# Kernel optimization log

Hardware: AMD Instinct MI355X
Metric: run time of the kernel (lower is better)

The kernel has to match this reference:

```python
import jax, jax.numpy as jnp
import numpy as np

NUM_HEADS = 16


def setup_inputs() -> dict:
    key = jax.random.key(0)
    k1, k2, k3 = jax.random.split(key, 3)
    B, S, D = 4, 2048, 1024
    hidden_states = jax.random.normal(k1, (B, S, D), dtype=jnp.float32)
    w_qkv = jax.random.normal(k2, (D, 3 * D), dtype=jnp.float32) * (1.0 / np.sqrt(D))
    w_out = jax.random.normal(k3, (D, D), dtype=jnp.float32) * (1.0 / np.sqrt(D))
    return {"hidden_states": hidden_states, "w_qkv": w_qkv, "w_out": w_out}


def reference(hidden_states, w_qkv, w_out):
    B, S, D = hidden_states.shape
    H = NUM_HEADS
    d = D // H
    # fused QKV projection: [B, S, 3D] -> [3, B, S, H, d]
    qkv = (hidden_states @ w_qkv).reshape(B, S, 3, H, d)
    q, k, v = jnp.moveaxis(qkv, 2, 0)  # each [B, S, H, d]
    scale = 1.0 / np.sqrt(d).astype(np.float32)
    scores = jnp.einsum("bqhd,bkhd->bhqk", q, k) * scale  # [B, H, S, S]
    attn = jax.nn.softmax(scores, axis=-1)
    ctx = jnp.einsum("bhqk,bkhd->bqhd", attn, v).reshape(B, S, D)
    return ctx @ w_out
```

## Files before the change

### kernel.cpp

```cpp
#include <hip/hip_runtime.h>
#include <hip/hip_bf16.h>
#include <math.h>

typedef __bf16 bf16;
typedef __bf16 bf16x4 __attribute__((ext_vector_type(4)));
typedef __bf16 bf16x8 __attribute__((ext_vector_type(8)));
typedef float  f32x4  __attribute__((ext_vector_type(4)));

#define B_  4
#define S_  2048
#define D_  1024
#define H_  16
#define DH  64
#define M_  (B_*S_)
#define BH_ (B_*H_)

#define QSCALE 0.18033688011112042f

__device__ __forceinline__ void glds16(const bf16* g, bf16* l) {
  __builtin_amdgcn_global_load_lds((const __attribute__((address_space(1))) void*)g,
                                   (__attribute__((address_space(3))) void*)l, 16, 0, 0);
}

__global__ __launch_bounds__(256) void prep(const float* __restrict__ hidden, bf16* __restrict__ hb,
                                            const float* __restrict__ wqkv, const float* __restrict__ wout,
                                            bf16* __restrict__ wqkvT, bf16* __restrict__ woutT) {
  int bx = blockIdx.x, tid = threadIdx.x;
  if (bx < 8192) {
    int i = (bx * 256 + tid) * 4;
    float4 v = *(const float4*)(hidden + i);
    bf16x4 o = { (bf16)v.x, (bf16)v.y, (bf16)v.z, (bf16)v.w };
    *(bf16x4*)(hb + i) = o;
    return;
  }
  __shared__ float tile[32][33];
  int t = bx - 8192;
  const float* in; bf16* out; int C, c0, r0;
  if (t < 96 * 32) { in = wqkv; out = wqkvT; C = 3072; c0 = (t % 96) * 32; r0 = (t / 96) * 32; }
  else { t -= 96 * 32;  in = wout; out = woutT; C = 1024; c0 = (t % 32) * 32; r0 = (t / 32) * 32; }
  int tx = tid & 31, ty = tid >> 5;
  #pragma unroll
  for (int i = ty; i < 32; i += 8) tile[i][tx] = in[(size_t)(r0 + i) * C + c0 + tx];
  __syncthreads();
  #pragma unroll
  for (int i = ty; i < 32; i += 8) out[(size_t)(c0 + i) * D_ + r0 + tx] = (bf16)tile[tx][i];
}

#define BM 256
#define BN 128
#define BK 64
#define NTILE (D_ / BK)
#define ATILE (BM * BK)
#define BTILE (BN * BK)

__device__ __forceinline__ void core256(const bf16* __restrict__ A, const bf16* __restrict__ Bt,
                                        int m0, int n0, bf16* As, bf16* Bs, int tid,
                                        f32x4 acc[4][4]) {
  const int wave = tid >> 6, lane = tid & 63, quad = lane >> 4, l16 = lane & 15;
  const int wm = (wave >> 1) * 64, wn = (wave & 1) * 64;
  const int lr8 = lane >> 3, lg = lane & 7;
  const int sg = ((lg ^ lr8) << 3);
  const bf16* gA = A  + (size_t)(m0 + lr8) * D_ + sg;
  const bf16* gB = Bt + (size_t)(n0 + lr8) * D_ + sg;
  const int swq  = ((quad ^ (l16 & 7)) << 3);
  const int swq4 = (((4 + quad) ^ (l16 & 7)) << 3);

#define STAGE_H1(slot, kt) do {                                                    \
    int koff = (kt) * BK;                                                          \
    bf16* a_d = As + (slot) * ATILE + wave * 2048;                                 \
    bf16* b_d = Bs + (slot) * BTILE + wave * 1024;                                 \
    glds16(gA + (size_t)(wave * 32 + 0) * D_ + koff, a_d + 0 * 512);               \
    glds16(gA + (size_t)(wave * 32 + 8) * D_ + koff, a_d + 1 * 512);               \
    glds16(gB + (size_t)(wave * 16 + 0) * D_ + koff, b_d + 0 * 512);               \
  } while (0)

#define STAGE_H2(slot, kt) do {                                                    \
    int koff = (kt) * BK;                                                          \
    bf16* a_d = As + (slot) * ATILE + wave * 2048;                                 \
    bf16* b_d = Bs + (slot) * BTILE + wave * 1024;                                 \
    glds16(gA + (size_t)(wave * 32 + 16) * D_ + koff, a_d + 2 * 512);              \
    glds16(gA + (size_t)(wave * 32 + 24) * D_ + koff, a_d + 3 * 512);              \
    glds16(gB + (size_t)(wave * 16 + 8)  * D_ + koff, b_d + 1 * 512);              \
  } while (0)

#define RDFRAG(slot, sw, af, bfr) do {                                             \
    const bf16* a_s = As + (slot) * ATILE;                                         \
    const bf16* b_s = Bs + (slot) * BTILE;                                         \
    _Pragma("unroll")                                                              \
    for (int i_ = 0; i_ < 4; i_++) af[i_]  = *(const bf16x8*)(a_s + (wm + i_ * 16 + l16) * 64 + (sw)); \
    _Pragma("unroll")                                                              \
    for (int j_ = 0; j_ < 4; j_++) bfr[j_] = *(const bf16x8*)(b_s + (wn + j_ * 16 + l16) * 64 + (sw)); \
  } while (0)

#define MFMA16(af, bfr) do {                                                       \
    _Pragma("unroll")                                                              \
    for (int i_ = 0; i_ < 4; i_++)                                                 \
      _Pragma("unroll")                                                            \
      for (int j_ = 0; j_ < 4; j_++)                                               \
        acc[i_][j_] = __builtin_amdgcn_mfma_f32_16x16x32_bf16(af[i_], bfr[j_], acc[i_][j_], 0, 0, 0); \
  } while (0)

#define PHASE256(slot, sw, STG, VMW, ENDBAR) do {                                  \
    bf16x8 af_[4], bf_[4];                                                         \
    RDFRAG(slot, sw, af_, bf_);                                                    \
    STG;                                                                           \
    __builtin_amdgcn_sched_barrier(0);                                             \
    __builtin_amdgcn_s_barrier();                                                  \
    asm volatile("s_waitcnt lgkmcnt(0)" ::: "memory");                             \
    __builtin_amdgcn_sched_barrier(0);                                             \
    __builtin_amdgcn_s_setprio(1);                                                 \
    MFMA16(af_, bf_);                                                              \
    __builtin_amdgcn_s_setprio(0);                                                 \
    __builtin_amdgcn_sched_barrier(0);                                             \
    VMW;                                                                           \
    if (ENDBAR) { __builtin_amdgcn_s_barrier(); __builtin_amdgcn_sched_barrier(0); } \
  } while (0)

  STAGE_H1(0, 0); STAGE_H2(0, 0); STAGE_H1(1, 1); STAGE_H2(1, 1);
  asm volatile("s_waitcnt vmcnt(6)" ::: "memory");
  __builtin_amdgcn_sched_barrier(0);
  __builtin_amdgcn_s_barrier();
  __builtin_amdgcn_sched_barrier(0);

  int scur = 0, snxt = 2;
  for (int t = 0; t < NTILE - 2; t++) {
    PHASE256(scur, swq,  STAGE_H1(snxt, t + 2), (void)0, 1);
    PHASE256(scur, swq4, STAGE_H2(snxt, t + 2),
             asm volatile("s_waitcnt vmcnt(6)" ::: "memory"), 1);
    scur = (scur == 2) ? 0 : scur + 1;
    snxt = (snxt == 2) ? 0 : snxt + 1;
  }
  PHASE256(scur, swq,  (void)0, (void)0, 1);
  PHASE256(scur, swq4, (void)0, asm volatile("s_waitcnt vmcnt(0)" ::: "memory"), 1);
  scur = (scur == 2) ? 0 : scur + 1;
  PHASE256(scur, swq,  (void)0, (void)0, 1);
  PHASE256(scur, swq4, (void)0, (void)0, 0);
#undef STAGE_H1
#undef STAGE_H2
#undef RDFRAG
#undef MFMA16
#undef PHASE256
}

__global__ __launch_bounds__(512, 1) void gemm_qkv(const bf16* __restrict__ A, const bf16* __restrict__ Bt,
                                                   bf16* __restrict__ Qb, bf16* __restrict__ Kb,
                                                   bf16* __restrict__ Vtb) {
  __shared__ __attribute__((aligned(16))) bf16 As[3 * ATILE];
  __shared__ __attribute__((aligned(16))) bf16 Bs[3 * BTILE];
  int tid = threadIdx.x;
  int m0 = blockIdx.y * BM, n0 = blockIdx.x * BN;
  f32x4 acc[4][4] = {};
  core256(A, Bt, m0, n0, As, Bs, tid, acc);
  int wave = tid >> 6, lane = tid & 63, quad = lane >> 4, l16 = lane & 15;
  int wm = (wave >> 1) * 64, wn = (wave & 1) * 64;
  int which = n0 >> 10;
  if (which == 2) {
    #pragma unroll
    for (int i = 0; i < 4; i++) {
      int mb = m0 + wm + i * 16 + quad * 4;
      int b = mb >> 11, s = mb & 2047;
      #pragma unroll
      for (int j = 0; j < 4; j++) {
        int n = n0 + wn + j * 16 + l16;
        int h = (n >> 6) & 15, dd = n & 63;
        bf16x4 v4 = { (bf16)acc[i][j][0], (bf16)acc[i][j][1], (bf16)acc[i][j][2], (bf16)acc[i][j][3] };
        *(bf16x4*)(Vtb + ((size_t)(b * H_ + h) * DH + dd) * S_ + s) = v4;
      }
    }
  } else {
    bf16* dst = (which == 0) ? Qb : Kb;
    float sc = (which == 0) ? QSCALE : 1.0f;
    #pragma unroll
    for (int i = 0; i < 4; i++) {
      #pragma unroll
      for (int j = 0; j < 4; j++) {
        int n = n0 + wn + j * 16 + l16;
        int h = (n >> 6) & 15, dd = n & 63;
        #pragma unroll
        for (int r = 0; r < 4; r++) {
          int m = m0 + wm + i * 16 + quad * 4 + r;
          int b = m >> 11, s = m & 2047;
          dst[(((size_t)(b * H_ + h)) * S_ + s) * DH + dd] = (bf16)(acc[i][j][r] * sc);
        }
      }
    }
  }
}

__global__ __launch_bounds__(512, 1) void gemm_out(const bf16* __restrict__ A, const bf16* __restrict__ Bt,
                                                   float* __restrict__ C) {
  __shared__ __attribute__((aligned(16))) bf16 As[3 * ATILE];
  __shared__ __attribute__((aligned(16))) bf16 Bs[3 * BTILE];
  int tid = threadIdx.x;
  int m0 = blockIdx.x * BM, n0 = blockIdx.y * BN;
  f32x4 acc[4][4] = {};
  core256(A, Bt, m0, n0, As, Bs, tid, acc);
  int wave = tid >> 6, lane = tid & 63, quad = lane >> 4, l16 = lane & 15;
  int wm = (wave >> 1) * 64, wn = (wave & 1) * 64;
  #pragma unroll
  for (int i = 0; i < 4; i++)
    #pragma unroll
    for (int j = 0; j < 4; j++) {
      int n = n0 + wn + j * 16 + l16;
      #pragma unroll
      for (int r = 0; r < 4; r++) {
        int m = m0 + wm + i * 16 + quad * 4 + r;
        C[(size_t)m * D_ + n] = acc[i][j][r];
      }
    }
}

#define NT  (S_ / 64)

#define KVSW(row, col) (((row) * 64) + ((col) ^ (((row) & 7) << 3)))
#define PSW(row, col)  (((row) * 32) + ((col) ^ ((((row) >> 1) & 3) << 3)))

__global__ __launch_bounds__(256, 4) void attn(const bf16* __restrict__ Qb, const bf16* __restrict__ Kb,
                                               const bf16* __restrict__ Vtb, bf16* __restrict__ ctx) {
  __shared__ __attribute__((aligned(16))) bf16 Ks[2][64 * 64];
  __shared__ __attribute__((aligned(16))) bf16 Vs[2][64 * 64];
  __shared__ __attribute__((aligned(16))) bf16 Ps[4][32 * 32];
  int tid = threadIdx.x;
  int wave = tid >> 6, lane = tid & 63, quad = lane >> 4, l16 = lane & 15;
  int bh = blockIdx.x;
  int b = bh >> 4, h = bh & 15;
  int q0 = blockIdx.y * 128 + wave * 32;
  const bf16* Qp = Qb  + (size_t)bh * S_ * DH;
  const bf16* Kp = Kb  + (size_t)bh * S_ * DH;
  const bf16* Vp = Vtb + (size_t)bh * DH * S_;

  int srow = tid >> 3, scc = (tid & 7) << 3;
  int swz = KVSW(srow, scc);

  bf16x8 qf[2][2];
  #pragma unroll
  for (int nq = 0; nq < 2; nq++)
    #pragma unroll
    for (int ks = 0; ks < 2; ks++)
      qf[nq][ks] = *(const bf16x8*)(Qp + (size_t)(q0 + nq * 16 + l16) * DH + ks * 32 + quad * 8);

  bf16 one1 = (bf16)1.0f;
  bf16x8 onesf = { one1, one1, one1, one1, one1, one1, one1, one1 };

  f32x4 o[2][4] = {};
  f32x4 oden[2] = {};

  {
    bf16x8 k0a = *(const bf16x8*)(Kp + (size_t)srow * DH + scc);
    bf16x8 k0b = *(const bf16x8*)(Kp + (size_t)(32 + srow) * DH + scc);
    bf16x8 v0a = *(const bf16x8*)(Vp + (size_t)srow * S_ + scc);
    bf16x8 v0b = *(const bf16x8*)(Vp + (size_t)(32 + srow) * S_ + scc);
    *(bf16x8*)(Ks[0] + swz)             = k0a;
    *(bf16x8*)(Ks[0] + swz + 32 * 64)   = k0b;
    *(bf16x8*)(Vs[0] + swz)             = v0a;
    *(bf16x8*)(Vs[0] + swz + 32 * 64)   = v0b;
  }

  for (int kt = 0; kt < NT; kt++) {
    int cur = kt & 1;
    __syncthreads();

    bf16x8 ka, kb2, va, vb;
    if (kt + 1 < NT) {
      const bf16* Kn = Kp + (size_t)(kt + 1) * 64 * DH;
      const bf16* Vn = Vp + (size_t)(kt + 1) * 64;
      ka  = *(const bf16x8*)(Kn + (size_t)srow * DH + scc);
      kb2 = *(const bf16x8*)(Kn + (size_t)(32 + srow) * DH + scc);
      va  = *(const bf16x8*)(Vn + (size_t)srow * S_ + scc);
      vb  = *(const bf16x8*)(Vn + (size_t)(32 + srow) * S_ + scc);
    }

    bf16x8 vf[4][2];
    #pragma unroll
    for (int td = 0; td < 4; td++)
      #pragma unroll
      for (int ks = 0; ks < 2; ks++)
        vf[td][ks] = *(const bf16x8*)(Vs[cur] + KVSW(td * 16 + l16, ks * 32 + quad * 8));

    #pragma unroll
    for (int hh = 0; hh < 2; hh++) {
      #pragma unroll
      for (int kq2 = 0; kq2 < 2; kq2++) {
        int kq = hh * 2 + kq2;
        bf16x8 kfr[2];
        #pragma unroll
        for (int ks = 0; ks < 2; ks++)
          kfr[ks] = *(const bf16x8*)(Ks[cur] + KVSW(kq * 16 + l16, ks * 32 + quad * 8));
        #pragma unroll
        for (int nq = 0; nq < 2; nq++) {
          f32x4 st = {};
          st = __builtin_amdgcn_mfma_f32_16x16x32_bf16(kfr[0], qf[nq][0], st, 0, 0, 0);
          st = __builtin_amdgcn_mfma_f32_16x16x32_bf16(kfr[1], qf[nq][1], st, 0, 0, 0);
          bf16x4 pk;
          #pragma unroll
          for (int r = 0; r < 4; r++) pk[r] = (bf16)__builtin_amdgcn_exp2f(st[r]);
          *(bf16x4*)(&Ps[wave][PSW(nq * 16 + l16, kq2 * 16 + quad * 4)]) = pk;
        }
      }
      #pragma unroll
      for (int nq = 0; nq < 2; nq++) {
        bf16x8 pf = *(const bf16x8*)(&Ps[wave][PSW(nq * 16 + l16, quad * 8)]);
        oden[nq] = __builtin_amdgcn_mfma_f32_16x16x32_bf16(pf, onesf, oden[nq], 0, 0, 0);
        #pragma unroll
        for (int td = 0; td < 4; td++)
          o[nq][td] = __builtin_amdgcn_mfma_f32_16x16x32_bf16(pf, vf[td][hh], o[nq][td], 0, 0, 0);
      }
    }

    if (kt + 1 < NT) {
      int nxt = cur ^ 1;
      *(bf16x8*)(Ks[nxt] + swz)           = ka;
      *(bf16x8*)(Ks[nxt] + swz + 32 * 64) = kb2;
      *(bf16x8*)(Vs[nxt] + swz)           = va;
      *(bf16x8*)(Vs[nxt] + swz + 32 * 64) = vb;
    }
  }

  #pragma unroll
  for (int nq = 0; nq < 2; nq++) {
    #pragma unroll
    for (int r = 0; r < 4; r++) {
      float inv = 1.0f / oden[nq][r];
      int q = q0 + nq * 16 + quad * 4 + r;
      #pragma unroll
      for (int td = 0; td < 4; td++) {
        int dd = td * 16 + l16;
        ctx[((size_t)(b * S_) + q) * D_ + h * DH + dd] = (bf16)(o[nq][td][r] * inv);
      }
    }
  }
}

extern "C" void kernel_launch(void* const* d_in, const int* in_sizes, int n_in,
                              void* d_out, int out_size, void* d_ws, size_t ws_size,
                              hipStream_t stream) {
  (void)in_sizes; (void)n_in; (void)out_size; (void)ws_size;
  const float* hidden = (const float*)d_in[0];
  const float* w_qkv  = (const float*)d_in[1];
  const float* w_out  = (const float*)d_in[2];
  float* out = (float*)d_out;

  char* ws = (char*)d_ws;
  size_t off = 0;
  bf16* hb    = (bf16*)(ws + off); off += (size_t)M_ * D_ * 2;
  bf16* wqkvT = (bf16*)(ws + off); off += (size_t)3 * D_ * D_ * 2;
  bf16* woutT = (bf16*)(ws + off); off += (size_t)D_ * D_ * 2;
  bf16* Qb    = (bf16*)(ws + off); off += (size_t)M_ * D_ * 2;
  bf16* Kb    = (bf16*)(ws + off); off += (size_t)M_ * D_ * 2;
  bf16* Vtb   = (bf16*)(ws + off); off += (size_t)M_ * D_ * 2;
  bf16* ctxb  = hb;

  prep<<<8192 + 96 * 32 + 32 * 32, 256, 0, stream>>>(hidden, hb, w_qkv, w_out, wqkvT, woutT);
  gemm_qkv<<<dim3(3 * D_ / BN, M_ / BM), 512, 0, stream>>>(hb, wqkvT, Qb, Kb, Vtb);
  attn<<<dim3(BH_, S_ / 128), 256, 0, stream>>>(Qb, Kb, Vtb, ctxb);
  gemm_out<<<dim3(M_ / BM, D_ / BN), 512, 0, stream>>>(ctxb, woutT, out);
}
```

Baseline: 258.5 us.

## Load K/V MFMA fragments directly from global memory instead of LDS staging

Removes the double-buffered LDS staging of K and V tiles in the attention kernel, along with the per-tile __syncthreads. Each wave now reads its K and V MFMA fragments straight from global memory, relying on L1/L2 caching since all four waves read the same tiles. This drops LDS traffic, barriers and LDS footprint, which could raise occupancy. The cost is that software prefetch is lost, global loads sit on the critical path, and redundant per-wave reads fall on the cache hierarchy.

```diff
diff --git a/kernel.cpp b/kernel.cpp
--- a/kernel.cpp
+++ b/kernel.cpp
@@ -211,14 +211,10 @@
 }
 
 #define NT  (S_ / 64)
-
-#define KVSW(row, col) (((row) * 64) + ((col) ^ (((row) & 7) << 3)))
 #define PSW(row, col)  (((row) * 32) + ((col) ^ ((((row) >> 1) & 3) << 3)))
 
 __global__ __launch_bounds__(256, 4) void attn(const bf16* __restrict__ Qb, const bf16* __restrict__ Kb,
                                                const bf16* __restrict__ Vtb, bf16* __restrict__ ctx) {
-  __shared__ __attribute__((aligned(16))) bf16 Ks[2][64 * 64];
-  __shared__ __attribute__((aligned(16))) bf16 Vs[2][64 * 64];
   __shared__ __attribute__((aligned(16))) bf16 Ps[4][32 * 32];
   int tid = threadIdx.x;
   int wave = tid >> 6, lane = tid & 63, quad = lane >> 4, l16 = lane & 15;
@@ -229,9 +225,6 @@
   const bf16* Kp = Kb  + (size_t)bh * S_ * DH;
   const bf16* Vp = Vtb + (size_t)bh * DH * S_;
 
-  int srow = tid >> 3, scc = (tid & 7) << 3;
-  int swz = KVSW(srow, scc);
-
   bf16x8 qf[2][2];
   #pragma unroll
   for (int nq = 0; nq < 2; nq++)
@@ -245,37 +238,16 @@
   f32x4 o[2][4] = {};
   f32x4 oden[2] = {};
 
-  {
-    bf16x8 k0a = *(const bf16x8*)(Kp + (size_t)srow * DH + scc);
-    bf16x8 k0b = *(const bf16x8*)(Kp + (size_t)(32 + srow) * DH + scc);
-    bf16x8 v0a = *(const bf16x8*)(Vp + (size_t)srow * S_ + scc);
-    bf16x8 v0b = *(const bf16x8*)(Vp + (size_t)(32 + srow) * S_ + scc);
-    *(bf16x8*)(Ks[0] + swz)             = k0a;
-    *(bf16x8*)(Ks[0] + swz + 32 * 64)   = k0b;
-    *(bf16x8*)(Vs[0] + swz)             = v0a;
-    *(bf16x8*)(Vs[0] + swz + 32 * 64)   = v0b;
-  }
-
   for (int kt = 0; kt < NT; kt++) {
-    int cur = kt & 1;
-    __syncthreads();
-
-    bf16x8 ka, kb2, va, vb;
-    if (kt + 1 < NT) {
-      const bf16* Kn = Kp + (size_t)(kt + 1) * 64 * DH;
-      const bf16* Vn = Vp + (size_t)(kt + 1) * 64;
-      ka  = *(const bf16x8*)(Kn + (size_t)srow * DH + scc);
-      kb2 = *(const bf16x8*)(Kn + (size_t)(32 + srow) * DH + scc);
-      va  = *(const bf16x8*)(Vn + (size_t)srow * S_ + scc);
-      vb  = *(const bf16x8*)(Vn + (size_t)(32 + srow) * S_ + scc);
-    }
+    const bf16* Kt = Kp + (size_t)kt * 64 * DH;
+    const bf16* Vt = Vp + (size_t)kt * 64;
 
     bf16x8 vf[4][2];
     #pragma unroll
     for (int td = 0; td < 4; td++)
       #pragma unroll
       for (int ks = 0; ks < 2; ks++)
-        vf[td][ks] = *(const bf16x8*)(Vs[cur] + KVSW(td * 16 + l16, ks * 32 + quad * 8));
+        vf[td][ks] = *(const bf16x8*)(Vt + (size_t)(td * 16 + l16) * S_ + ks * 32 + quad * 8);
 
     #pragma unroll
     for (int hh = 0; hh < 2; hh++) {
@@ -285,7 +257,7 @@
         bf16x8 kfr[2];
         #pragma unroll
         for (int ks = 0; ks < 2; ks++)
-          kfr[ks] = *(const bf16x8*)(Ks[cur] + KVSW(kq * 16 + l16, ks * 32 + quad * 8));
+          kfr[ks] = *(const bf16x8*)(Kt + (size_t)(kq * 16 + l16) * DH + ks * 32 + quad * 8);
         #pragma unroll
         for (int nq = 0; nq < 2; nq++) {
           f32x4 st = {};
@@ -306,14 +278,6 @@
           o[nq][td] = __builtin_amdgcn_mfma_f32_16x16x32_bf16(pf, vf[td][hh], o[nq][td], 0, 0, 0);
       }
     }
-
-    if (kt + 1 < NT) {
-      int nxt = cur ^ 1;
-      *(bf16x8*)(Ks[nxt] + swz)           = ka;
-      *(bf16x8*)(Ks[nxt] + swz + 32 * 64) = kb2;
-      *(bf16x8*)(Vs[nxt] + swz)           = va;
-      *(bf16x8*)(Vs[nxt] + swz + 32 * 64) = vb;
-    }
   }
 
   #pragma unroll
```

New measurement: 404.7 us. +56.6%, slower.
